# Kernel optimization log

Hardware: AMD Instinct MI355X
Metric: run time of the kernel (lower is better)

The kernel has to match this reference:

```python
import jax, jax.numpy as jnp
import numpy as np
import math

D_MODEL = 512
SLOPE = 0.5  # slope_init, not trainable


def setup_inputs() -> dict:
    key = jax.random.key(0)
    k1, k2, k3, k4 = jax.random.split(key, 4)
    B, S, D = 4, 4096, D_MODEL
    x = jax.random.normal(k1, (B, S, D), dtype=jnp.float32)
    # nn.Linear(d, d): weight is [d, d]; query_key weight used as x @ W (no transpose, bias unused)
    lim = 1.0 / math.sqrt(D)
    W_qk = jax.random.uniform(k2, (D, D), jnp.float32, -lim, lim)
    W_v = jax.random.uniform(k3, (D, D), jnp.float32, -lim, lim)
    b_v = jax.random.uniform(k4, (D,), jnp.float32, -lim, lim)
    return {"x": x, "W_qk": W_qk, "W_v": W_v, "b_v": b_v}


def reference(x, W_qk, W_v, b_v):
    B, S, D = x.shape
    scale = 1.0 / math.sqrt(D)
    # scores[b,i,j] = (x @ W_qk @ x^T) * scale   (torch: x @ weight @ x.transpose)
    scores = jnp.einsum('bid,de,bje->bij', x, W_qk, x) * scale
    # ALiBi bias: (j - i) * slope
    i = jnp.arange(S, dtype=x.dtype)[:, None]
    j = jnp.arange(S, dtype=x.dtype)[None, :]
    scores = scores + (j - i) * jnp.asarray(SLOPE, x.dtype)
    # causal mask: strict upper triangle -> -inf
    causal = j > i  # [S, S] bool
    scores = jnp.where(causal, -jnp.inf, scores)
    attn = jax.nn.softmax(scores, axis=-1)
    # value_linear: x @ W_v^T + b_v (standard nn.Linear)
    v = jnp.einsum('bjd,ed->bje', x, W_v) + b_v
    return jnp.einsum('bij,bje->bie', attn, v)
```

## Files before the change

kernel.cpp:

```cpp
#include <hip/hip_runtime.h>
#include <math.h>

#define D_MODEL 512
#define SEQ     4096
#define BATCH   4
#define BS      (BATCH * SEQ)

typedef __attribute__((ext_vector_type(8))) short  short8;
typedef __attribute__((ext_vector_type(4))) float  float4v;

#define GAS __attribute__((address_space(1)))
#define LAS __attribute__((address_space(3)))

__device__ __forceinline__ void gld_lds16(const void* g, void* l) {
  __builtin_amdgcn_global_load_lds((const GAS unsigned int*)g,
                                   (LAS unsigned int*)l, 16, 0, 0);
}

__device__ __forceinline__ unsigned short bf16r(float f) {
  unsigned int u = __builtin_bit_cast(unsigned int, f);
  u += 0x7fffu + ((u >> 16) & 1u);
  return (unsigned short)(u >> 16);
}

__device__ __forceinline__ uint4 pack8(float4 a, float4 b) {
  uint4 o;
  o.x = bf16r(a.x) | ((unsigned)bf16r(a.y) << 16);
  o.y = bf16r(a.z) | ((unsigned)bf16r(a.w) << 16);
  o.z = bf16r(b.x) | ((unsigned)bf16r(b.y) << 16);
  o.w = bf16r(b.z) | ((unsigned)bf16r(b.w) << 16);
  return o;
}

__global__ __launch_bounds__(256) void cvt_w(const float* __restrict__ Wqk,
                                             unsigned short* __restrict__ Wqkt,
                                             const float* __restrict__ Wv,
                                             unsigned short* __restrict__ Wvb) {
  if (blockIdx.x < 64) {
    __shared__ float tile[64][65];
    const int bx = blockIdx.x & 7;
    const int by = blockIdx.x >> 3;
    const int tx = threadIdx.x & 63;
    const int ty = threadIdx.x >> 6;
    for (int r = ty; r < 64; r += 4)
      tile[r][tx] = Wqk[(size_t)(by * 64 + r) * D_MODEL + bx * 64 + tx];
    __syncthreads();
    for (int r = ty; r < 64; r += 4)
      Wqkt[(size_t)(bx * 64 + r) * D_MODEL + by * 64 + tx] = bf16r(tile[tx][r]);
  } else {
    const int idx = ((blockIdx.x - 64) * 256 + threadIdx.x) * 8;
    const float4 a = *(const float4*)(Wv + idx);
    const float4 b = *(const float4*)(Wv + idx + 4);
    *(uint4*)(Wvb + idx) = pack8(a, b);
  }
}

template <bool QP>
__device__ __forceinline__ void gemm_path(const float* __restrict__ x,
                                          const unsigned short* __restrict__ Wgt,
                                          const float* __restrict__ bias,
                                          unsigned short* __restrict__ xb,
                                          unsigned short* __restrict__ C,
                                          int a0, float scale,
                                          unsigned short* smem) {
  unsigned short* Ws = smem;
  unsigned short* As = smem + 32768;

  const int t    = threadIdx.x;
  const int w    = t >> 6;
  const int lane = t & 63;
  const int q    = lane >> 4;
  const int c    = lane & 15;
  const int wbase = w * 128;
  const int sw   = c & 7;

  const int arow = t >> 2;
  const int acb  = (t & 3) * 16;

  constexpr int NI = QP ? 8 : 4;
  constexpr int NJ = QP ? 4 : 8;

  float4v acc[NI][NJ];
#pragma unroll
  for (int i = 0; i < NI; ++i)
#pragma unroll
    for (int j = 0; j < NJ; ++j) acc[i][j] = (float4v){0.f, 0.f, 0.f, 0.f};

  for (int k0 = 0; k0 < D_MODEL; k0 += 64) {
#pragma unroll
    for (int it = 0; it < 16; ++it) {
      const int idx = it * 256 + t;
      const int r   = idx >> 3;
      const int s   = idx & 7;
      gld_lds16(Wgt + (size_t)r * D_MODEL + k0 + ((s ^ (r & 7)) << 3),
                &Ws[idx * 8]);
    }
    {
      const float* xg = x + (size_t)(a0 + arow) * D_MODEL + k0 + acb;
      const float4 f0 = *(const float4*)(xg + 0);
      const float4 f1 = *(const float4*)(xg + 4);
      const float4 f2 = *(const float4*)(xg + 8);
      const float4 f3 = *(const float4*)(xg + 12);
      const uint4 u0 = pack8(f0, f1);
      const uint4 u1 = pack8(f2, f3);
      const int s0 = (t & 3) * 2;
      const int rk = arow & 7;
      *(uint4*)&As[arow * 64 + ((s0 ^ rk) << 3)]       = u0;
      *(uint4*)&As[arow * 64 + (((s0 + 1) ^ rk) << 3)] = u1;
      if (QP) {
        unsigned short* xo = xb + (size_t)(a0 + arow) * D_MODEL + k0 + acb;
        *(uint4*)xo       = u0;
        *(uint4*)(xo + 8) = u1;
      }
    }
    __syncthreads();

#pragma unroll
    for (int kc = 0; kc < 2; ++kc) {
      const int slot = ((kc * 4 + q) ^ sw) * 8;
      short8 af[NI], bf[NJ];
#pragma unroll
      for (int i = 0; i < NI; ++i) {
        const unsigned short* src = QP ? &Ws[(wbase + i * 16 + c) * 64 + slot]
                                       : &As[(i * 16 + c) * 64 + slot];
        af[i] = *(const short8*)src;
      }
#pragma unroll
      for (int j = 0; j < NJ; ++j) {
        const unsigned short* src = QP ? &As[(j * 16 + c) * 64 + slot]
                                       : &Ws[(wbase + j * 16 + c) * 64 + slot];
        bf[j] = *(const short8*)src;
      }
#pragma unroll
      for (int i = 0; i < NI; ++i)
#pragma unroll
        for (int j = 0; j < NJ; ++j)
          acc[i][j] = __builtin_amdgcn_mfma_f32_16x16x32_bf16(af[i], bf[j], acc[i][j], 0, 0, 0);
    }
    __syncthreads();
  }

  if (QP) {
    constexpr int LD = 520;
#pragma unroll
    for (int j = 0; j < NJ; ++j) {
      const int row = j * 16 + c;
#pragma unroll
      for (int i = 0; i < NI; ++i) {
        uint2 pkt;
        pkt.x = (unsigned)bf16r(scale * acc[i][j][0]) |
                ((unsigned)bf16r(scale * acc[i][j][1]) << 16);
        pkt.y = (unsigned)bf16r(scale * acc[i][j][2]) |
                ((unsigned)bf16r(scale * acc[i][j][3]) << 16);
        *(uint2*)&smem[row * LD + wbase + i * 16 + 4 * q] = pkt;
      }
    }
    __syncthreads();
#pragma unroll
    for (int it = 0; it < 16; ++it) {
      const int idx = it * 256 + t;
      const int row = idx >> 6;
      const int ch  = idx & 63;
      *(uint4*)&C[(size_t)(a0 + row) * D_MODEL + ch * 8] =
          *(const uint4*)&smem[row * LD + ch * 8];
    }
  } else {
    constexpr int LD = 72;
#pragma unroll
    for (int j = 0; j < NJ; ++j) {
      const int dim = wbase + j * 16 + c;
      const float bvv = bias[dim];
#pragma unroll
      for (int i = 0; i < NI; ++i) {
        uint2 pkt;
        pkt.x = (unsigned)bf16r(acc[i][j][0] + bvv) |
                ((unsigned)bf16r(acc[i][j][1] + bvv) << 16);
        pkt.y = (unsigned)bf16r(acc[i][j][2] + bvv) |
                ((unsigned)bf16r(acc[i][j][3] + bvv) << 16);
        *(uint2*)&smem[dim * LD + i * 16 + 4 * q] = pkt;
      }
    }
    __syncthreads();
#pragma unroll
    for (int it = 0; it < 16; ++it) {
      const int idx = it * 256 + t;
      const int dim = idx >> 3;
      const int ch  = idx & 7;
      *(uint4*)&C[(size_t)dim * BS + a0 + ch * 8] =
          *(const uint4*)&smem[dim * LD + ch * 8];
    }
  }
}

__global__ __launch_bounds__(256, 2) void qv_gemm(const float* __restrict__ x,
                                                  const unsigned short* __restrict__ Wqkt,
                                                  const unsigned short* __restrict__ Wvb,
                                                  const float* __restrict__ bv,
                                                  unsigned short* __restrict__ xb,
                                                  unsigned short* __restrict__ Qb,
                                                  unsigned short* __restrict__ Vt,
                                                  float scale) {
  __shared__ unsigned short smem[36864];
  if (blockIdx.x < 256)
    gemm_path<true>(x, Wqkt, nullptr, xb, Qb, blockIdx.x * 64, scale, smem);
  else
    gemm_path<false>(x, Wvb, bv, nullptr, Vt, (blockIdx.x - 256) * 64, 1.0f, smem);
}

__global__ __launch_bounds__(128) void attn_tile(const unsigned short* __restrict__ Q,
                                                 const unsigned short* __restrict__ Kx,
                                                 const unsigned short* __restrict__ Vt,
                                                 float* __restrict__ out) {
  constexpr int PLD = 72;
  __shared__ unsigned short pls[16 * PLD];
  __shared__ float lm[2][16], ls[2][16];

  const int t    = threadIdx.x;
  const int h    = t >> 6;
  const int lane = t & 63;
  const int q    = lane >> 4;
  const int c    = lane & 15;

  const int tile = ((blockIdx.x & 7) << 7) + (blockIdx.x >> 3);
  const int r0   = tile << 4;
  const int b    = r0 >> 12;
  const int i0   = r0 & (SEQ - 1);
  const int jb   = i0 - 48;

  short8 qf[16];
  {
    const unsigned short* qp = Q + (size_t)(r0 + c) * D_MODEL + q * 8;
#pragma unroll
    for (int ch = 0; ch < 16; ++ch) qf[ch] = *(const short8*)(qp + ch * 32);
  }

  float4v sacc[2];
  sacc[0] = (float4v){0.f, 0.f, 0.f, 0.f};
  sacc[1] = (float4v){0.f, 0.f, 0.f, 0.f};
#pragma unroll
  for (int s = 0; s < 2; ++s) {
    const int sj = 2 * h + s;
    if (jb + 16 * sj + 15 < 0) continue;
    int krow = jb + 16 * sj + c;
    if (krow < 0) krow = 0;
    const unsigned short* kr = Kx + ((size_t)(b << 12) + krow) * D_MODEL + q * 8;
    float4v sv = sacc[s];
#pragma unroll
    for (int ch = 0; ch < 16; ++ch)
      sv = __builtin_amdgcn_mfma_f32_16x16x32_bf16(qf[ch], *(const short8*)(kr + ch * 32), sv, 0, 0, 0);
    sacc[s] = sv;
  }

  const unsigned short* vbase = Vt + (size_t)(h * 256 + c) * BS + (b << 12);
  const bool ch0 = (jb + 31 >= 0);
  short8 vf0[16];
  if (ch0) {
    int kk = jb + q * 8;
    if (kk < 0) kk = 0;
    const unsigned short* vb = vbase + kk;
#pragma unroll
    for (int dt = 0; dt < 16; ++dt) vf0[dt] = *(const short8*)(vb + (size_t)dt * 16 * BS);
  }

  float tmax[4] = {-1e30f, -1e30f, -1e30f, -1e30f};
#pragma unroll
  for (int s = 0; s < 2; ++s)
#pragma unroll
    for (int tt = 0; tt < 4; ++tt) {
      const int jl = jb + 16 * (2 * h + s) + c;
      const int il = i0 + 4 * q + tt;
      float sv = sacc[s][tt];
      sv = (jl < 0 || jl > il) ? -1e30f : sv + 0.5f * (float)(jl - il);
      sacc[s][tt] = sv;
      tmax[tt] = fmaxf(tmax[tt], sv);
    }
#pragma unroll
  for (int tt = 0; tt < 4; ++tt) {
    float v = tmax[tt];
    v = fmaxf(v, __shfl_xor(v, 1, 64));
    v = fmaxf(v, __shfl_xor(v, 2, 64));
    v = fmaxf(v, __shfl_xor(v, 4, 64));
    v = fmaxf(v, __shfl_xor(v, 8, 64));
    tmax[tt] = v;
  }
  if (c == 0) {
#pragma unroll
    for (int tt = 0; tt < 4; ++tt) lm[h][4 * q + tt] = tmax[tt];
  }
  __syncthreads();

  float m[4];
#pragma unroll
  for (int tt = 0; tt < 4; ++tt)
    m[tt] = fmaxf(lm[0][4 * q + tt], lm[1][4 * q + tt]);

  float rsum[4] = {0.f, 0.f, 0.f, 0.f};
#pragma unroll
  for (int s = 0; s < 2; ++s)
#pragma unroll
    for (int tt = 0; tt < 4; ++tt) {
      const float p = __expf(sacc[s][tt] - m[tt]);
      rsum[tt] += p;
      pls[(4 * q + tt) * PLD + (2 * h + s) * 16 + c] = bf16r(p);
    }
#pragma unroll
  for (int tt = 0; tt < 4; ++tt) {
    float v = rsum[tt];
    v += __shfl_xor(v, 1, 64);
    v += __shfl_xor(v, 2, 64);
    v += __shfl_xor(v, 4, 64);
    v += __shfl_xor(v, 8, 64);
    rsum[tt] = v;
  }
  if (c == 0) {
#pragma unroll
    for (int tt = 0; tt < 4; ++tt) ls[h][4 * q + tt] = rsum[tt];
  }
  __syncthreads();

  float l[4];
#pragma unroll
  for (int tt = 0; tt < 4; ++tt)
    l[tt] = ls[0][4 * q + tt] + ls[1][4 * q + tt];

  float4v oacc[16];
#pragma unroll
  for (int dt = 0; dt < 16; ++dt) oacc[dt] = (float4v){0.f, 0.f, 0.f, 0.f};

  if (ch0) {
    const short8 pa = *(const short8*)&pls[c * PLD + q * 8];
#pragma unroll
    for (int dt = 0; dt < 16; ++dt)
      oacc[dt] = __builtin_amdgcn_mfma_f32_16x16x32_bf16(pa, vf0[dt], oacc[dt], 0, 0, 0);
  }
  {
    const short8 pa = *(const short8*)&pls[c * PLD + 32 + q * 8];
    int kk = jb + 32 + q * 8;
    if (kk < 0) kk = 0;
    const unsigned short* vb = vbase + kk;
#pragma unroll
    for (int dt = 0; dt < 16; ++dt) {
      const short8 vf = *(const short8*)(vb + (size_t)dt * 16 * BS);
      oacc[dt] = __builtin_amdgcn_mfma_f32_16x16x32_bf16(pa, vf, oacc[dt], 0, 0, 0);
    }
  }

  float inv[4];
#pragma unroll
  for (int tt = 0; tt < 4; ++tt) inv[tt] = 1.0f / l[tt];
#pragma unroll
  for (int dt = 0; dt < 16; ++dt)
#pragma unroll
    for (int tt = 0; tt < 4; ++tt)
      out[(size_t)(r0 + 4 * q + tt) * D_MODEL + h * 256 + dt * 16 + c] =
          oacc[dt][tt] * inv[tt];
}

extern "C" void kernel_launch(void* const* d_in, const int* in_sizes, int n_in,
                              void* d_out, int out_size, void* d_ws,
                              size_t ws_size, hipStream_t stream) {
  const float* x   = (const float*)d_in[0];
  const float* Wqk = (const float*)d_in[1];
  const float* Wv  = (const float*)d_in[2];
  const float* bv  = (const float*)d_in[3];
  float* out = (float*)d_out;

  unsigned short* xb   = (unsigned short*)d_ws;
  unsigned short* Qb   = xb + (size_t)BS * D_MODEL;
  unsigned short* Vt   = Qb + (size_t)BS * D_MODEL;
  unsigned short* Wqkt = Vt + (size_t)BS * D_MODEL;
  unsigned short* Wvb  = Wqkt + (size_t)D_MODEL * D_MODEL;

  const float scale = 1.0f / sqrtf((float)D_MODEL);

  cvt_w<<<dim3(192), dim3(256), 0, stream>>>(Wqk, Wqkt, Wv, Wvb);
  qv_gemm<<<dim3(512), dim3(256), 0, stream>>>(x, Wqkt, Wvb, bv, xb, Qb, Vt, scale);
  attn_tile<<<dim3(BS / 16), dim3(128), 0, stream>>>(Qb, xb, Vt, out);
}
```

Baseline: 133.2 us.

## Split attention tile across four waves and stage Q tile in LDS

Raises the attention block from two to four waves. Each wave now handles one 16-key score subtile and a 128-wide slice of the output instead of two subtiles and a 256-wide slice. The Q tile is loaded cooperatively into shared memory once and read back from there, rather than each wave holding all 16 Q fragments in registers. This cuts per-thread register pressure and adds latency hiding, at the cost of an extra barrier, more LDS use, and a four-way cross-wave reduction for the softmax max and sum.

```diff
diff --git a/kernel.cpp b/kernel.cpp
--- a/kernel.cpp
+++ b/kernel.cpp
@@ -207,13 +207,15 @@
     gemm_path<false>(x, Wvb, bv, nullptr, Vt, (blockIdx.x - 256) * 64, 1.0f, smem);
 }
 
-__global__ __launch_bounds__(128) void attn_tile(const unsigned short* __restrict__ Q,
+__global__ __launch_bounds__(256) void attn_tile(const unsigned short* __restrict__ Q,
                                                  const unsigned short* __restrict__ Kx,
                                                  const unsigned short* __restrict__ Vt,
                                                  float* __restrict__ out) {
+  constexpr int QLD = 520;
   constexpr int PLD = 72;
+  __shared__ unsigned short qls[16 * QLD];
   __shared__ unsigned short pls[16 * PLD];
-  __shared__ float lm[2][16], ls[2][16];
+  __shared__ float lm[4][16], ls[4][16];
 
   const int t    = threadIdx.x;
   const int h    = t >> 6;
@@ -227,56 +229,51 @@
   const int i0   = r0 & (SEQ - 1);
   const int jb   = i0 - 48;
 
-  short8 qf[16];
+#pragma unroll
+  for (int i = 0; i < 4; ++i) {
+    const int idx = i * 256 + t;
+    const int row = idx >> 6;
+    const int ch  = idx & 63;
+    *(uint4*)&qls[row * QLD + ch * 8] =
+        *(const uint4*)&Q[(size_t)(r0 + row) * D_MODEL + ch * 8];
+  }
+  __syncthreads();
+
+  float4v sacc = (float4v){0.f, 0.f, 0.f, 0.f};
   {
-    const unsigned short* qp = Q + (size_t)(r0 + c) * D_MODEL + q * 8;
-#pragma unroll
-    for (int ch = 0; ch < 16; ++ch) qf[ch] = *(const short8*)(qp + ch * 32);
-  }
-
-  float4v sacc[2];
-  sacc[0] = (float4v){0.f, 0.f, 0.f, 0.f};
-  sacc[1] = (float4v){0.f, 0.f, 0.f, 0.f};
-#pragma unroll
-  for (int s = 0; s < 2; ++s) {
-    const int sj = 2 * h + s;
-    if (jb + 16 * sj + 15 < 0) continue;
-    int krow = jb + 16 * sj + c;
-    if (krow < 0) krow = 0;
-    const unsigned short* kr = Kx + ((size_t)(b << 12) + krow) * D_MODEL + q * 8;
-    float4v sv = sacc[s];
-#pragma unroll
-    for (int ch = 0; ch < 16; ++ch)
-      sv = __builtin_amdgcn_mfma_f32_16x16x32_bf16(qf[ch], *(const short8*)(kr + ch * 32), sv, 0, 0, 0);
-    sacc[s] = sv;
-  }
-
-  const unsigned short* vbase = Vt + (size_t)(h * 256 + c) * BS + (b << 12);
+    const int sj = h;
+    if (jb + 16 * sj + 15 >= 0) {
+      int krow = jb + 16 * sj + c;
+      if (krow < 0) krow = 0;
+      const unsigned short* kr = Kx + ((size_t)(b << 12) + krow) * D_MODEL + q * 8;
+#pragma unroll
+      for (int ch = 0; ch < 16; ++ch) {
+        const short8 qf = *(const short8*)&qls[c * QLD + ch * 32 + q * 8];
+        sacc = __builtin_amdgcn_mfma_f32_16x16x32_bf16(qf, *(const short8*)(kr + ch * 32), sacc, 0, 0, 0);
+      }
+    }
+  }
+
+  const unsigned short* vbase = Vt + (size_t)(h * 128 + c) * BS + (b << 12);
   const bool ch0 = (jb + 31 >= 0);
-  short8 vf0[16];
+  short8 vf0[8];
   if (ch0) {
     int kk = jb + q * 8;
     if (kk < 0) kk = 0;
     const unsigned short* vb = vbase + kk;
 #pragma unroll
-    for (int dt = 0; dt < 16; ++dt) vf0[dt] = *(const short8*)(vb + (size_t)dt * 16 * BS);
-  }
-
-  float tmax[4] = {-1e30f, -1e30f, -1e30f, -1e30f};
-#pragma unroll
-  for (int s = 0; s < 2; ++s)
-#pragma unroll
-    for (int tt = 0; tt < 4; ++tt) {
-      const int jl = jb + 16 * (2 * h + s) + c;
-      const int il = i0 + 4 * q + tt;
-      float sv = sacc[s][tt];
-      sv = (jl < 0 || jl > il) ? -1e30f : sv + 0.5f * (float)(jl - il);
-      sacc[s][tt] = sv;
-      tmax[tt] = fmaxf(tmax[tt], sv);
-    }
+    for (int dt = 0; dt < 8; ++dt) vf0[dt] = *(const short8*)(vb + (size_t)dt * 16 * BS);
+  }
+
+  float tmax[4];
 #pragma unroll
   for (int tt = 0; tt < 4; ++tt) {
-    float v = tmax[tt];
+    const int jl = jb + 16 * h + c;
+    const int il = i0 + 4 * q + tt;
+    float sv = sacc[tt];
+    sv = (jl < 0 || jl > il) ? -1e30f : sv + 0.5f * (float)(jl - il);
+    sacc[tt] = sv;
+    float v = sv;
     v = fmaxf(v, __shfl_xor(v, 1, 64));
     v = fmaxf(v, __shfl_xor(v, 2, 64));
     v = fmaxf(v, __shfl_xor(v, 4, 64));
@@ -289,23 +286,14 @@
   }
   __syncthreads();
 
-  float m[4];
-#pragma unroll
-  for (int tt = 0; tt < 4; ++tt)
-    m[tt] = fmaxf(lm[0][4 * q + tt], lm[1][4 * q + tt]);
-
-  float rsum[4] = {0.f, 0.f, 0.f, 0.f};
-#pragma unroll
-  for (int s = 0; s < 2; ++s)
-#pragma unroll
-    for (int tt = 0; tt < 4; ++tt) {
-      const float p = __expf(sacc[s][tt] - m[tt]);
-      rsum[tt] += p;
-      pls[(4 * q + tt) * PLD + (2 * h + s) * 16 + c] = bf16r(p);
-    }
+  float rsum[4];
 #pragma unroll
   for (int tt = 0; tt < 4; ++tt) {
-    float v = rsum[tt];
+    const float m = fmaxf(fmaxf(lm[0][4 * q + tt], lm[1][4 * q + tt]),
+                          fmaxf(lm[2][4 * q + tt], lm[3][4 * q + tt]));
+    const float p = __expf(sacc[tt] - m);
+    pls[(4 * q + tt) * PLD + h * 16 + c] = bf16r(p);
+    float v = p;
     v += __shfl_xor(v, 1, 64);
     v += __shfl_xor(v, 2, 64);
     v += __shfl_xor(v, 4, 64);
@@ -321,16 +309,17 @@
   float l[4];
 #pragma unroll
   for (int tt = 0; tt < 4; ++tt)
-    l[tt] = ls[0][4 * q + tt] + ls[1][4 * q + tt];
-
-  float4v oacc[16];
-#pragma unroll
-  for (int dt = 0; dt < 16; ++dt) oacc[dt] = (float4v){0.f, 0.f, 0.f, 0.f};
+    l[tt] = ls[0][4 * q + tt] + ls[1][4 * q + tt] +
+            ls[2][4 * q + tt] + ls[3][4 * q + tt];
+
+  float4v oacc[8];
+#pragma unroll
+  for (int dt = 0; dt < 8; ++dt) oacc[dt] = (float4v){0.f, 0.f, 0.f, 0.f};
 
   if (ch0) {
     const short8 pa = *(const short8*)&pls[c * PLD + q * 8];
 #pragma unroll
-    for (int dt = 0; dt < 16; ++dt)
+    for (int dt = 0; dt < 8; ++dt)
       oacc[dt] = __builtin_amdgcn_mfma_f32_16x16x32_bf16(pa, vf0[dt], oacc[dt], 0, 0, 0);
   }
   {
@@ -339,7 +328,7 @@
     if (kk < 0) kk = 0;
     const unsigned short* vb = vbase + kk;
 #pragma unroll
-    for (int dt = 0; dt < 16; ++dt) {
+    for (int dt = 0; dt < 8; ++dt) {
       const short8 vf = *(const short8*)(vb + (size_t)dt * 16 * BS);
       oacc[dt] = __builtin_amdgcn_mfma_f32_16x16x32_bf16(pa, vf, oacc[dt], 0, 0, 0);
     }
@@ -349,10 +338,10 @@
 #pragma unroll
   for (int tt = 0; tt < 4; ++tt) inv[tt] = 1.0f / l[tt];
 #pragma unroll
-  for (int dt = 0; dt < 16; ++dt)
+  for (int dt = 0; dt < 8; ++dt)
 #pragma unroll
     for (int tt = 0; tt < 4; ++tt)
-      out[(size_t)(r0 + 4 * q + tt) * D_MODEL + h * 256 + dt * 16 + c] =
+      out[(size_t)(r0 + 4 * q + tt) * D_MODEL + h * 128 + dt * 16 + c] =
           oacc[dt][tt] * inv[tt];
 }
 
@@ -375,5 +364,5 @@
 
   cvt_w<<<dim3(192), dim3(256), 0, stream>>>(Wqk, Wqkt, Wv, Wvb);
   qv_gemm<<<dim3(512), dim3(256), 0, stream>>>(x, Wqkt, Wvb, bv, xb, Qb, Vt, scale);
-  attn_tile<<<dim3(BS / 16), dim3(128), 0, stream>>>(Qb, xb, Vt, out);
-}
+  attn_tile<<<dim3(BS / 16), dim3(256), 0, stream>>>(Qb, xb, Vt, out);
+}
```

Result: no change. 130.7 us (-1.8%).
